# Kernel tuning notes

Hardware: AMD Instinct MI355X
Metric: run time of the kernel (lower is better)

## Reference

```python
import jax, jax.numpy as jnp
import numpy as np

H = 4096
NUM_HEADS = 32
D = 128
SEQ_LEN = 1024
CTX = 4096


def setup_inputs() -> dict:
    key = jax.random.key(0)
    k1, k2, k3, k4 = jax.random.split(key, 4)
    X = jax.random.normal(k1, (SEQ_LEN, H), dtype=jnp.float32)
    # Linear weight [out=3H, in=H]; scale ~1/sqrt(H) so attention logits are O(1)
    W = jax.random.normal(k2, (3 * H, H), dtype=jnp.float32) * (1.0 / np.sqrt(H))
    cache_K = jax.random.normal(k3, (1, CTX, NUM_HEADS, D), dtype=jnp.float32)
    cache_V = jax.random.normal(k4, (1, CTX, NUM_HEADS, D), dtype=jnp.float32)
    return {"X": X, "W": W, "cache_K": cache_K, "cache_V": cache_V}


def reference(X, W, cache_K, cache_V):
    seq_len, h = X.shape
    nh, d = cache_K.shape[2], cache_K.shape[3]
    # fused QKV projection (Linear, no bias): X @ W^T -> [seq_len, 3H]
    qkv = X @ W.T
    q, k, v = jnp.split(qkv, 3, axis=1)
    q = q.reshape(1, seq_len, nh, d)
    k = k.reshape(1, seq_len, nh, d)
    v = v.reshape(1, seq_len, nh, d)
    # concat KV cache along the sequence dim (cache_K[:, :P] with P = full cache)
    k_full = jnp.concatenate([cache_K, k], axis=1)  # [1, ctx+seq, nh, d]
    v_full = jnp.concatenate([cache_V, v], axis=1)
    scale = 1.0 / np.sqrt(d)
    # scores: [1, nh, seq_q, kv_len]
    scores = jnp.einsum("bqhd,bkhd->bhqk", q, k_full) * scale
    weights = jax.nn.softmax(scores, axis=-1)
    out = jnp.einsum("bhqk,bkhd->bqhd", weights, v_full)  # [1, seq, nh, d]
    return out.reshape(seq_len, h)
```

## Files before the change

### kernel.cpp

```cpp
#include <hip/hip_runtime.h>
#include <hip/hip_bf16.h>
#include <stdint.h>

#define H_DIM 4096
#define NH 32
#define HD 128
#define SEQ 1024
#define CTX 4096
#define KVL (CTX + SEQ)
#define W3H (3 * H_DIM)
#define ATTN_SCALE 0.08838834764831845f

typedef short short8 __attribute__((ext_vector_type(8)));
typedef float f32x4 __attribute__((ext_vector_type(4)));

#define GLOAD_LDS16(g, l)                                             \
  __builtin_amdgcn_global_load_lds(                                   \
      (const __attribute__((address_space(1))) void*)(g),             \
      (__attribute__((address_space(3))) void*)(l), 16, 0, 0)

__device__ __forceinline__ unsigned short f2b(float f) {
  union { float f; unsigned u; } v; v.f = f;
  return (unsigned short)((v.u + 0x7FFFu + ((v.u >> 16) & 1u)) >> 16);
}
__device__ __forceinline__ float b2f(unsigned short u) {
  union { unsigned u; float f; } v; v.u = ((unsigned)u) << 16;
  return v.f;
}

__global__ void k_cvt2(const float* __restrict__ X, const float* __restrict__ W,
                       unsigned short* __restrict__ Xb, unsigned short* __restrict__ Wb) {
  const int nx = SEQ * H_DIM / 4;
  const int nw = W3H * H_DIM / 4;
  int i = blockIdx.x * 256 + threadIdx.x;
  const float* s;
  unsigned short* d;
  int j;
  if (i < nx) { s = X; d = Xb; j = i; }
  else { j = i - nx; if (j >= nw) return; s = W; d = Wb; }
  float4 v = reinterpret_cast<const float4*>(s)[j];
  ushort4 o;
  o.x = f2b(v.x); o.y = f2b(v.y); o.z = f2b(v.z); o.w = f2b(v.w);
  reinterpret_cast<ushort4*>(d)[j] = o;
}

#define GBM 256
#define GBN 256
#define GBK 64
#define GNKT (H_DIM / GBK)
__global__ __launch_bounds__(512, 2) void k_gemm_qkv(
    const unsigned short* __restrict__ A,
    const unsigned short* __restrict__ B,
    unsigned short* __restrict__ C) {
  __shared__ __align__(16) char Lds[131072];
  const int tid = threadIdx.x;
  const int lane = tid & 63;
  const int wid = tid >> 6;
  const int wm = wid >> 2;
  const int wn = wid & 3;
  const int lq = lane >> 4;
  const int lr = lane & 15;

  const int id = blockIdx.x;
  const int wg = (id & 7) * 24 + (id >> 3);
  const int bm = wg & 3;
  const int bn = wg >> 2;

  const int sel = 8 * ((lane & 7) ^ (lane >> 3));

#define GSTAGE(t, buf)                                                         \
  {                                                                            \
    _Pragma("unroll") for (int i = 0; i < 4; ++i) {                            \
      int c = wid * 4 + i;                                                     \
      GLOAD_LDS16(A + (size_t)(bm * GBM + c * 8 + (lane >> 3)) * H_DIM +       \
                      (t) * GBK + sel,                                         \
                  Lds + (buf) * 65536 + c * 1024);                             \
      GLOAD_LDS16(B + (size_t)(bn * GBN + c * 8 + (lane >> 3)) * H_DIM +       \
                      (t) * GBK + sel,                                         \
                  Lds + (buf) * 65536 + 32768 + c * 1024);                     \
    }                                                                          \
  }

  f32x4 acc[8][4] = {};

#define GCOMP(buf)                                                             \
  {                                                                            \
    _Pragma("unroll") for (int kk = 0; kk < 2; ++kk) {                         \
      short8 af[8], bfr[4];                                                    \
      _Pragma("unroll") for (int m = 0; m < 8; ++m)                            \
        af[m] = *reinterpret_cast<const short8*>(                              \
            Lds + (buf) * 65536 + (wm * 128 + m * 16 + lr) * 128 +             \
            16 * ((kk * 4 + lq) ^ (lr & 7)));                                  \
      _Pragma("unroll") for (int n = 0; n < 4; ++n)                            \
        bfr[n] = *reinterpret_cast<const short8*>(                             \
            Lds + (buf) * 65536 + 32768 + (wn * 64 + n * 16 + lr) * 128 +      \
            16 * ((kk * 4 + lq) ^ (lr & 7)));                                  \
      __builtin_amdgcn_s_setprio(1);                                           \
      _Pragma("unroll") for (int m = 0; m < 8; ++m)                            \
        _Pragma("unroll") for (int n = 0; n < 4; ++n)                          \
          acc[m][n] = __builtin_amdgcn_mfma_f32_16x16x32_bf16(                 \
              af[m], bfr[n], acc[m][n], 0, 0, 0);                              \
      __builtin_amdgcn_s_setprio(0);                                           \
    }                                                                          \
  }

  GSTAGE(0, 0);
  GSTAGE(1, 1);
  asm volatile("s_waitcnt vmcnt(8)" ::: "memory");
  __builtin_amdgcn_sched_barrier(0);
  __builtin_amdgcn_s_barrier();
  __builtin_amdgcn_sched_barrier(0);

  for (int t = 0; t < GNKT; ++t) {
    const int cur = t & 1;
    GCOMP(cur);
    __builtin_amdgcn_sched_barrier(0);
    __builtin_amdgcn_s_barrier();
    __builtin_amdgcn_sched_barrier(0);
    if (t + 2 < GNKT) {
      GSTAGE(t + 2, cur);
      asm volatile("s_waitcnt vmcnt(8)" ::: "memory");
    } else {
      asm volatile("s_waitcnt vmcnt(0)" ::: "memory");
    }
    __builtin_amdgcn_sched_barrier(0);
    __builtin_amdgcn_s_barrier();
    __builtin_amdgcn_sched_barrier(0);
  }

  const int r0 = bm * GBM + wm * 128 + lq * 4;
  const int c0 = bn * GBN + wn * 64 + lr;
#pragma unroll
  for (int m = 0; m < 8; ++m)
#pragma unroll
    for (int n = 0; n < 4; ++n)
#pragma unroll
      for (int r = 0; r < 4; ++r)
        C[(size_t)(r0 + m * 16 + r) * W3H + c0 + n * 16] = f2b(acc[m][n][r]);
#undef GSTAGE
#undef GCOMP
}

__global__ void k_build_k(const float* __restrict__ cK, const unsigned short* __restrict__ QKV,
                          unsigned short* __restrict__ Kb) {
  int idx = (blockIdx.x * 256 + threadIdx.x) * 4;
  if (idx >= NH * KVL * HD) return;
  int h = idx / (KVL * HD);
  int rem = idx % (KVL * HD);
  int kv = rem / HD;
  int d = rem % HD;
  ushort4 o;
  if (kv < CTX) {
    float4 v = *reinterpret_cast<const float4*>(cK + ((size_t)kv * NH + h) * HD + d);
    o.x = f2b(v.x); o.y = f2b(v.y); o.z = f2b(v.z); o.w = f2b(v.w);
  } else {
    o = *reinterpret_cast<const ushort4*>(QKV + (size_t)(kv - CTX) * W3H + H_DIM + h * HD + d);
  }
  *reinterpret_cast<ushort4*>(Kb + idx) = o;
}

__global__ void k_build_vt(const float* __restrict__ cV, const unsigned short* __restrict__ QKV,
                           unsigned short* __restrict__ Vt) {
  __shared__ unsigned short T[HD][66];
  const int h = blockIdx.y;
  const int kt = blockIdx.x;
  const int t = threadIdx.x;
#pragma unroll
  for (int e = 0; e < 8; ++e) {
    int idx = (t + e * 256) * 4;
    int kvl = idx >> 7;
    int d = idx & 127;
    int kv = kt * 64 + kvl;
    unsigned short a, b, c, w;
    if (kv < CTX) {
      float4 v = *reinterpret_cast<const float4*>(cV + ((size_t)kv * NH + h) * HD + d);
      a = f2b(v.x); b = f2b(v.y); c = f2b(v.z); w = f2b(v.w);
    } else {
      ushort4 u = *reinterpret_cast<const ushort4*>(QKV + (size_t)(kv - CTX) * W3H + 2 * H_DIM + h * HD + d);
      a = u.x; b = u.y; c = u.z; w = u.w;
    }
    T[d][kvl] = a; T[d + 1][kvl] = b; T[d + 2][kvl] = c; T[d + 3][kvl] = w;
  }
  __syncthreads();
#pragma unroll
  for (int e = 0; e < 8; ++e) {
    int idx = (t + e * 256) * 4;
    int d = idx >> 6;
    int kv0 = idx & 63;
    ushort4 o;
    o.x = T[d][kv0]; o.y = T[d][kv0 + 1]; o.z = T[d][kv0 + 2]; o.w = T[d][kv0 + 3];
    *reinterpret_cast<ushort4*>(Vt + ((size_t)h * HD + d) * KVL + kt * 64 + kv0) = o;
  }
}

#define KVT 64
#define NT (KVL / KVT)
#define NT2 (NT / 2)
__global__ __launch_bounds__(256, 2) void k_attn(
    const unsigned short* __restrict__ QKV,
    const unsigned short* __restrict__ Kb,
    const unsigned short* __restrict__ Vt,
    float* __restrict__ A0,
    float* __restrict__ A1,
    float* __restrict__ Mp,
    float* __restrict__ Lp) {
  __shared__ unsigned short Ks[2][KVT * HD];
  __shared__ unsigned short Vs[2][KVT * HD];
  const int tid = threadIdx.x, lane = tid & 63, wid = tid >> 6;
  const int g = lane >> 4;
  const int qi = lane & 15;
  const int id = blockIdx.x;
  const int xcd = id & 7, slot = id >> 3;
  const int h = xcd * 4 + (slot >> 4);
  const int rem = slot & 15;
  const int qt = rem >> 1;
  const int split = rem & 1;
  const int kt0 = split * NT2;
  const int q0 = qt * 128 + wid * 32;

  short8 qf[2][4];
#pragma unroll
  for (int hf = 0; hf < 2; ++hf)
#pragma unroll
    for (int c = 0; c < 4; ++c) {
      short8 q = *reinterpret_cast<const short8*>(
          QKV + (size_t)(q0 + hf * 16 + qi) * W3H + h * HD + c * 32 + g * 8);
      short8 t;
#pragma unroll
      for (int j = 0; j < 8; ++j) t[j] = (short)f2b(b2f((unsigned short)q[j]) * ATTN_SCALE);
      qf[hf][c] = t;
    }

  float m_r[2] = {-1e30f, -1e30f}, l_r[2] = {0.f, 0.f};
  f32x4 acc_o[2][8] = {};

  const char* Kh = (const char*)(Kb + (size_t)h * KVL * HD);
  const char* Vh = (const char*)(Vt + (size_t)h * HD * KVL);

#define STAGE_K(t, b)                                                          \
  {                                                                            \
    _Pragma("unroll") for (int i = 0; i < 4; ++i) {                            \
      int c = wid * 4 + i;                                                     \
      int krow = c * 4 + (lane >> 4);                                          \
      int klcb = (16 * (lane & 15)) ^ ((krow & 7) << 4);                       \
      GLOAD_LDS16(Kh + (size_t)((t) * KVT + krow) * 256 + klcb,                \
                  (char*)Ks[b] + c * 1024);                                    \
    }                                                                          \
  }
#define STAGE_V(t, b)                                                          \
  {                                                                            \
    _Pragma("unroll") for (int i = 0; i < 4; ++i) {                            \
      int c = wid * 4 + i;                                                     \
      int vrow = c * 8 + (lane >> 3);                                          \
      int vlcb = (16 * (lane & 7)) ^ ((vrow & 7) << 4);                        \
      GLOAD_LDS16(Vh + (size_t)vrow * (KVL * 2) + (size_t)(t) * 128 + vlcb,    \
                  (char*)Vs[b] + c * 1024);                                    \
    }                                                                          \
  }
#define QKT(buf, S)                                                            \
  {                                                                            \
    _Pragma("unroll") for (int n = 0; n < 4; ++n) {                            \
      S[0][n] = (f32x4){0.f, 0.f, 0.f, 0.f};                                   \
      S[1][n] = (f32x4){0.f, 0.f, 0.f, 0.f};                                   \
    }                                                                          \
    __builtin_amdgcn_s_setprio(1);                                             \
    _Pragma("unroll") for (int n = 0; n < 4; ++n) {                            \
      int row = n * 16 + qi;                                                   \
      _Pragma("unroll") for (int c = 0; c < 4; ++c) {                          \
        int cb = (c * 32 + g * 8) * 2;                                         \
        short8 kf = *reinterpret_cast<const short8*>(                          \
            (const char*)Ks[buf] + row * 256 + (cb ^ ((row & 7) << 4)));       \
        S[0][n] = __builtin_amdgcn_mfma_f32_16x16x32_bf16(kf, qf[0][c], S[0][n], 0, 0, 0); \
        S[1][n] = __builtin_amdgcn_mfma_f32_16x16x32_bf16(kf, qf[1][c], S[1][n], 0, 0, 0); \
      }                                                                        \
    }                                                                          \
    __builtin_amdgcn_s_setprio(0);                                             \
  }

  const int i0 = ((2 * (g & 1) + 0) * 16 + qi) * 4;
  const int i1 = ((2 * (g & 1) + 1) * 16 + qi) * 4;

#define SMPV(S, vb)                                                            \
  {                                                                            \
    float p[2][4][4];                                                          \
    int okv = 1;                                                               \
    float tmax[2];                                                             \
    _Pragma("unroll") for (int hf = 0; hf < 2; ++hf) {                         \
      float t0 = S[hf][0][0];                                                  \
      _Pragma("unroll") for (int n = 0; n < 4; ++n)                            \
        _Pragma("unroll") for (int r = 0; r < 4; ++r)                          \
          t0 = fmaxf(t0, S[hf][n][r]);                                         \
      t0 = fmaxf(t0, __shfl_xor(t0, 16, 64));                                  \
      t0 = fmaxf(t0, __shfl_xor(t0, 32, 64));                                  \
      tmax[hf] = t0;                                                           \
      okv &= (t0 <= m_r[hf] + 8.0f);                                           \
    }                                                                          \
    if (!__all(okv)) {                                                         \
      _Pragma("unroll") for (int hf = 0; hf < 2; ++hf) {                       \
        float mn = fmaxf(m_r[hf], tmax[hf]);                                   \
        float alpha = __expf(m_r[hf] - mn);                                    \
        l_r[hf] *= alpha;                                                      \
        m_r[hf] = mn;                                                          \
        _Pragma("unroll") for (int nd = 0; nd < 8; ++nd) acc_o[hf][nd] *= alpha; \
      }                                                                        \
    }                                                                          \
    _Pragma("unroll") for (int hf = 0; hf < 2; ++hf) {                         \
      float sum = 0.f;                                                         \
      _Pragma("unroll") for (int n = 0; n < 4; ++n)                            \
        _Pragma("unroll") for (int r = 0; r < 4; ++r) {                        \
          p[hf][n][r] = __expf(S[hf][n][r] - m_r[hf]);                         \
          sum += p[hf][n][r];                                                  \
        }                                                                      \
      sum += __shfl_xor(sum, 16, 64);                                          \
      sum += __shfl_xor(sum, 32, 64);                                          \
      l_r[hf] += sum;                                                          \
    }                                                                          \
    unsigned pr[2][4][2];                                                      \
    _Pragma("unroll") for (int hf = 0; hf < 2; ++hf)                           \
      _Pragma("unroll") for (int n = 0; n < 4; ++n)                            \
        _Pragma("unroll") for (int rr = 0; rr < 2; ++rr) {                     \
          union { __hip_bfloat162 b; unsigned u; } cv;                         \
          cv.b = __float22bfloat162_rn(                                        \
              make_float2(p[hf][n][2 * rr], p[hf][n][2 * rr + 1]));            \
          pr[hf][n][rr] = cv.u;                                                \
        }                                                                      \
    _Pragma("unroll") for (int kc = 0; kc < 2; ++kc) {                         \
      short8 pv[2];                                                            \
      _Pragma("unroll") for (int hf = 0; hf < 2; ++hf) {                       \
        int a0 = __builtin_amdgcn_ds_bpermute(i0, (int)pr[hf][2 * kc][0]);     \
        int b0 = __builtin_amdgcn_ds_bpermute(i0, (int)pr[hf][2 * kc + 1][0]); \
        int a1 = __builtin_amdgcn_ds_bpermute(i0, (int)pr[hf][2 * kc][1]);     \
        int b1 = __builtin_amdgcn_ds_bpermute(i0, (int)pr[hf][2 * kc + 1][1]); \
        int a2 = __builtin_amdgcn_ds_bpermute(i1, (int)pr[hf][2 * kc][0]);     \
        int b2 = __builtin_amdgcn_ds_bpermute(i1, (int)pr[hf][2 * kc + 1][0]); \
        int a3 = __builtin_amdgcn_ds_bpermute(i1, (int)pr[hf][2 * kc][1]);     \
        int b3 = __builtin_amdgcn_ds_bpermute(i1, (int)pr[hf][2 * kc + 1][1]); \
        union { int i[4]; short8 s8; } u;                                      \
        u.i[0] = (g < 2) ? a0 : b0;                                            \
        u.i[1] = (g < 2) ? a1 : b1;                                            \
        u.i[2] = (g < 2) ? a2 : b2;                                            \
        u.i[3] = (g < 2) ? a3 : b3;                                            \
        pv[hf] = u.s8;                                                         \
      }                                                                        \
      __builtin_amdgcn_s_setprio(1);                                           \
      _Pragma("unroll") for (int nd = 0; nd < 8; ++nd) {                       \
        int row = nd * 16 + qi;                                                \
        int cb = kc * 64 + g * 16;                                             \
        short8 vf = *reinterpret_cast<const short8*>(                          \
            (const char*)Vs[vb] + row * 128 + (cb ^ ((row & 7) << 4)));        \
        acc_o[0][nd] = __builtin_amdgcn_mfma_f32_16x16x32_bf16(vf, pv[0], acc_o[0][nd], 0, 0, 0); \
        acc_o[1][nd] = __builtin_amdgcn_mfma_f32_16x16x32_bf16(vf, pv[1], acc_o[1][nd], 0, 0, 0); \
      }                                                                        \
      __builtin_amdgcn_s_setprio(0);                                           \
    }                                                                          \
  }

#define BODY(t, SC, SN)                                                        \
  {                                                                            \
    const int cur = (t) & 1;                                                   \
    if ((t) + 2 < NT2) STAGE_K(kt0 + (t) + 2, cur);                            \
    if ((t) + 1 < NT2) QKT(cur ^ 1, SN);                                       \
    SMPV(SC, cur);                                                             \
    __syncthreads();                                                           \
    if ((t) + 2 < NT2) STAGE_V(kt0 + (t) + 2, cur);                            \
  }

  STAGE_K(kt0, 0);
  STAGE_V(kt0, 0);
  STAGE_K(kt0 + 1, 1);
  STAGE_V(kt0 + 1, 1);
  __syncthreads();

  f32x4 sA[2][4], sB[2][4];
  QKT(0, sA);

  for (int tt = 0; tt < NT2; tt += 2) {
    BODY(tt, sA, sB);
    BODY(tt + 1, sB, sA);
  }

  float* Op = split ? A1 : A0;
#pragma unroll
  for (int hf = 0; hf < 2; ++hf) {
    float* orow = Op + (size_t)(q0 + hf * 16 + qi) * H_DIM + h * HD;
#pragma unroll
    for (int nd = 0; nd < 8; ++nd)
      *reinterpret_cast<float4*>(orow + nd * 16 + g * 4) =
          *reinterpret_cast<const float4*>(&acc_o[hf][nd]);
    if (g == 0) {
      int q = q0 + hf * 16 + qi;
      Mp[split * (NH * SEQ) + h * SEQ + q] = m_r[hf];
      Lp[split * (NH * SEQ) + h * SEQ + q] = l_r[hf];
    }
  }
#undef STAGE_K
#undef STAGE_V
#undef QKT
#undef SMPV
#undef BODY
}

__global__ void k_combine(const float* __restrict__ A1, const float* __restrict__ Mp,
                          const float* __restrict__ Lp, float* __restrict__ out) {
  int i4 = blockIdx.x * 256 + threadIdx.x;
  int q = i4 >> 10;
  int c4 = i4 & 1023;
  int h = c4 >> 5;
  float m0 = Mp[h * SEQ + q], m1 = Mp[NH * SEQ + h * SEQ + q];
  float l0 = Lp[h * SEQ + q], l1 = Lp[NH * SEQ + h * SEQ + q];
  float M = fmaxf(m0, m1);
  float w0 = __expf(m0 - M), w1 = __expf(m1 - M);
  float inv = 1.0f / (w0 * l0 + w1 * l1);
  float4 a0 = reinterpret_cast<const float4*>(out)[i4];
  float4 a1 = reinterpret_cast<const float4*>(A1)[i4];
  float4 o;
  o.x = (w0 * a0.x + w1 * a1.x) * inv;
  o.y = (w0 * a0.y + w1 * a1.y) * inv;
  o.z = (w0 * a0.z + w1 * a1.z) * inv;
  o.w = (w0 * a0.w + w1 * a1.w) * inv;
  reinterpret_cast<float4*>(out)[i4] = o;
}

extern "C" void kernel_launch(void* const* d_in, const int* in_sizes, int n_in,
                              void* d_out, int out_size, void* d_ws, size_t ws_size,
                              hipStream_t stream) {
  const float* X = (const float*)d_in[0];
  const float* W = (const float*)d_in[1];
  const float* cK = (const float*)d_in[2];
  const float* cV = (const float*)d_in[3];
  float* out = (float*)d_out;
  char* ws = (char*)d_ws;

  unsigned short* Xb = (unsigned short*)(ws);
  float* Mp = (float*)(ws);
  float* Lp = (float*)(ws + (256 << 10));
  unsigned short* QKVb = (unsigned short*)(ws + ((size_t)8 << 20));
  unsigned short* Wb = (unsigned short*)(ws + ((size_t)32 << 20));
  unsigned short* Kb = (unsigned short*)(ws + ((size_t)32 << 20));
  unsigned short* Vt = (unsigned short*)(ws + ((size_t)72 << 20));
  float* A1 = (float*)(ws + ((size_t)112 << 20));

  int ncvt = (SEQ * H_DIM + W3H * H_DIM) / 4;
  k_cvt2<<<(ncvt + 255) / 256, 256, 0, stream>>>(X, W, Xb, Wb);

  k_gemm_qkv<<<(SEQ / GBM) * (W3H / GBN), 512, 0, stream>>>(Xb, Wb, QKVb);

  k_build_k<<<(NH * KVL * HD / 4) / 256, 256, 0, stream>>>(cK, QKVb, Kb);
  dim3 gv(KVL / 64, NH);
  k_build_vt<<<gv, 256, 0, stream>>>(cV, QKVb, Vt);

  k_attn<<<SEQ / 128 * NH * 2, 256, 0, stream>>>(QKVb, Kb, Vt, out, A1, Mp, Lp);
  k_combine<<<(SEQ * H_DIM / 4) / 256, 256, 0, stream>>>(A1, Mp, Lp, out);
}
```

Before: 359.5 us.

## Interleave QKV GEMM global loads with MFMA phases in a four-phase schedule

Restructures the QKV projection GEMM main loop into four phases per K tile. Each phase loads a slice of A fragments and issues a quarter of the next-stage global-to-LDS loads, with A prefetched one tile ahead and B two tiles ahead, so memory traffic overlaps MFMA work instead of arriving in one burst. Launch bounds drop from two to one block per CU, giving each thread more registers for the held B fragments. The cost is more barriers per tile and lower occupancy, and correctness depends on the buffer reuse and waitcnt ordering being right.

```diff
diff --git a/kernel.cpp b/kernel.cpp
--- a/kernel.cpp
+++ b/kernel.cpp
@@ -48,7 +48,7 @@
 #define GBN 256
 #define GBK 64
 #define GNKT (H_DIM / GBK)
-__global__ __launch_bounds__(512, 2) void k_gemm_qkv(
+__global__ __launch_bounds__(512, 1) void k_gemm_qkv(
     const unsigned short* __restrict__ A,
     const unsigned short* __restrict__ B,
     unsigned short* __restrict__ C) {
@@ -66,66 +66,92 @@
   const int bm = wg & 3;
   const int bn = wg >> 2;
 
+  const unsigned short* Abase = A + (size_t)(bm * GBM) * H_DIM;
+  const unsigned short* Bbase = B + (size_t)(bn * GBN) * H_DIM;
   const int sel = 8 * ((lane & 7) ^ (lane >> 3));
-
-#define GSTAGE(t, buf)                                                         \
-  {                                                                            \
-    _Pragma("unroll") for (int i = 0; i < 4; ++i) {                            \
-      int c = wid * 4 + i;                                                     \
-      GLOAD_LDS16(A + (size_t)(bm * GBM + c * 8 + (lane >> 3)) * H_DIM +       \
+  const int srow = lane >> 3;
+
+#define GUNIT_A(t, h, b)                                                       \
+  {                                                                            \
+    _Pragma("unroll") for (int j = 0; j < 2; ++j) {                            \
+      int c = wid * 2 + j;                                                     \
+      GLOAD_LDS16(Abase + (size_t)((h) * 128 + c * 8 + srow) * H_DIM +         \
                       (t) * GBK + sel,                                         \
-                  Lds + (buf) * 65536 + c * 1024);                             \
-      GLOAD_LDS16(B + (size_t)(bn * GBN + c * 8 + (lane >> 3)) * H_DIM +       \
+                  Lds + (b) * 65536 + (h) * 16384 + c * 1024);                 \
+    }                                                                          \
+  }
+#define GUNIT_B(t, h, b)                                                       \
+  {                                                                            \
+    _Pragma("unroll") for (int j = 0; j < 2; ++j) {                            \
+      int c = wid * 2 + j;                                                     \
+      GLOAD_LDS16(Bbase + (size_t)((h) * 128 + c * 8 + srow) * H_DIM +         \
                       (t) * GBK + sel,                                         \
-                  Lds + (buf) * 65536 + 32768 + c * 1024);                     \
+                  Lds + (b) * 65536 + 32768 + (h) * 16384 + c * 1024);         \
     }                                                                          \
   }
 
   f32x4 acc[8][4] = {};
 
-#define GCOMP(buf)                                                             \
-  {                                                                            \
-    _Pragma("unroll") for (int kk = 0; kk < 2; ++kk) {                         \
-      short8 af[8], bfr[4];                                                    \
-      _Pragma("unroll") for (int m = 0; m < 8; ++m)                            \
-        af[m] = *reinterpret_cast<const short8*>(                              \
-            Lds + (buf) * 65536 + (wm * 128 + m * 16 + lr) * 128 +             \
+#define GPHASE(T, q)                                                           \
+  {                                                                            \
+    const int cb_ = ((T) & 1) * 65536;                                         \
+    short8 af[2][2];                                                           \
+    _Pragma("unroll") for (int mm = 0; mm < 2; ++mm)                           \
+      _Pragma("unroll") for (int kk = 0; kk < 2; ++kk)                         \
+        af[mm][kk] = *reinterpret_cast<const short8*>(                         \
+            Lds + cb_ + (wm * 128 + ((q) * 2 + mm) * 16 + lr) * 128 +          \
             16 * ((kk * 4 + lq) ^ (lr & 7)));                                  \
+    if ((q) == 0) {                                                            \
       _Pragma("unroll") for (int n = 0; n < 4; ++n)                            \
-        bfr[n] = *reinterpret_cast<const short8*>(                             \
-            Lds + (buf) * 65536 + 32768 + (wn * 64 + n * 16 + lr) * 128 +      \
-            16 * ((kk * 4 + lq) ^ (lr & 7)));                                  \
-      __builtin_amdgcn_s_setprio(1);                                           \
-      _Pragma("unroll") for (int m = 0; m < 8; ++m)                            \
+        _Pragma("unroll") for (int kk = 0; kk < 2; ++kk)                       \
+          bfr[n][kk] = *reinterpret_cast<const short8*>(                       \
+              Lds + cb_ + 32768 + (wn * 64 + n * 16 + lr) * 128 +              \
+              16 * ((kk * 4 + lq) ^ (lr & 7)));                                \
+    }                                                                          \
+    if ((q) == 0 && (T) + 1 < GNKT) GUNIT_A((T) + 1, 0, ((T) + 1) & 1);        \
+    if ((q) == 1 && (T) + 1 < GNKT) GUNIT_A((T) + 1, 1, ((T) + 1) & 1);        \
+    if ((q) == 2 && (T) + 2 < GNKT) GUNIT_B((T) + 2, 0, (T) & 1);              \
+    if ((q) == 3 && (T) + 2 < GNKT) GUNIT_B((T) + 2, 1, (T) & 1);              \
+    if ((q) == 3) {                                                            \
+      if ((T) + 2 < GNKT) {                                                    \
+        asm volatile("s_waitcnt vmcnt(4)" ::: "memory");                       \
+      } else {                                                                 \
+        asm volatile("s_waitcnt vmcnt(0)" ::: "memory");                       \
+      }                                                                        \
+    }                                                                          \
+    __builtin_amdgcn_sched_barrier(0);                                         \
+    __builtin_amdgcn_s_barrier();                                              \
+    asm volatile("s_waitcnt lgkmcnt(0)" ::: "memory");                         \
+    __builtin_amdgcn_sched_barrier(0);                                         \
+    __builtin_amdgcn_s_setprio(1);                                             \
+    _Pragma("unroll") for (int kk = 0; kk < 2; ++kk)                           \
+      _Pragma("unroll") for (int mm = 0; mm < 2; ++mm)                         \
         _Pragma("unroll") for (int n = 0; n < 4; ++n)                          \
-          acc[m][n] = __builtin_amdgcn_mfma_f32_16x16x32_bf16(                 \
-              af[m], bfr[n], acc[m][n], 0, 0, 0);                              \
-      __builtin_amdgcn_s_setprio(0);                                           \
-    }                                                                          \
-  }
-
-  GSTAGE(0, 0);
-  GSTAGE(1, 1);
-  asm volatile("s_waitcnt vmcnt(8)" ::: "memory");
+          acc[(q) * 2 + mm][n] = __builtin_amdgcn_mfma_f32_16x16x32_bf16(      \
+              af[mm][kk], bfr[n][kk], acc[(q) * 2 + mm][n], 0, 0, 0);          \
+    __builtin_amdgcn_s_setprio(0);                                             \
+    __builtin_amdgcn_sched_barrier(0);                                         \
+    __builtin_amdgcn_s_barrier();                                              \
+    __builtin_amdgcn_sched_barrier(0);                                         \
+  }
+
+  GUNIT_A(0, 0, 0);
+  GUNIT_A(0, 1, 0);
+  GUNIT_B(0, 0, 0);
+  GUNIT_B(0, 1, 0);
+  GUNIT_B(1, 0, 1);
+  GUNIT_B(1, 1, 1);
+  asm volatile("s_waitcnt vmcnt(4)" ::: "memory");
   __builtin_amdgcn_sched_barrier(0);
   __builtin_amdgcn_s_barrier();
   __builtin_amdgcn_sched_barrier(0);
 
-  for (int t = 0; t < GNKT; ++t) {
-    const int cur = t & 1;
-    GCOMP(cur);
-    __builtin_amdgcn_sched_barrier(0);
-    __builtin_amdgcn_s_barrier();
-    __builtin_amdgcn_sched_barrier(0);
-    if (t + 2 < GNKT) {
-      GSTAGE(t + 2, cur);
-      asm volatile("s_waitcnt vmcnt(8)" ::: "memory");
-    } else {
-      asm volatile("s_waitcnt vmcnt(0)" ::: "memory");
-    }
-    __builtin_amdgcn_sched_barrier(0);
-    __builtin_amdgcn_s_barrier();
-    __builtin_amdgcn_sched_barrier(0);
+  for (int T = 0; T < GNKT; ++T) {
+    short8 bfr[4][2];
+    GPHASE(T, 0);
+    GPHASE(T, 1);
+    GPHASE(T, 2);
+    GPHASE(T, 3);
   }
 
   const int r0 = bm * GBM + wm * 128 + lq * 4;
@@ -137,8 +163,9 @@
 #pragma unroll
       for (int r = 0; r < 4; ++r)
         C[(size_t)(r0 + m * 16 + r) * W3H + c0 + n * 16] = f2b(acc[m][n][r]);
-#undef GSTAGE
-#undef GCOMP
+#undef GUNIT_A
+#undef GUNIT_B
+#undef GPHASE
 }
 
 __global__ void k_build_k(const float* __restrict__ cK, const unsigned short* __restrict__ QKV,
```

Result: faster. 337.1 us (-6.2%).
